# Optimization experiments

Measured on AMD Instinct MI355X. Metric: run time of the kernel, lower is better.

## Reference

```python
import jax, jax.numpy as jnp
import numpy as np

B, T, TAU = 4, 512, 512
D_MODEL = 1024  # in_dim == out_dim (required: pos embedding dim out_dim feeds pos_proj with in_size=in_dim)
H, D = 16, 64
LN_EPS = 1e-5


def rel_shift(x):
    # x: [B, T, L, H] -> Transformer-XL relative shift
    b, t, l, h = x.shape
    x = jnp.pad(x, ((0, 0), (0, 0), (1, 0), (0, 0)))  # pad j-dim front
    x = x.reshape(b, l + 1, t, h)[:, 1:, :, :]
    return x.reshape(b, t, l, h)


def setup_inputs() -> dict:
    key = jax.random.key(0)
    ks = jax.random.split(key, 7)
    s = 0.02
    return {
        "inputs": jax.random.normal(ks[0], (B, T, D_MODEL), jnp.float32),
        "memory": jax.random.normal(ks[1], (B, TAU, D_MODEL), jnp.float32),
        "w_qkv": jax.random.normal(ks[2], (3 * H * D, D_MODEL), jnp.float32) * s,
        "w_pos": jax.random.normal(ks[3], (H * D, D_MODEL), jnp.float32) * s,
        "w_out": jax.random.normal(ks[4], (D_MODEL, H * D), jnp.float32) * s,
        "uvar": jax.random.normal(ks[5], (H, D), jnp.float32) * s,
        "vvar": jax.random.normal(ks[6], (H, D), jnp.float32) * s,
        "ln_gamma": jnp.ones((D_MODEL,), jnp.float32),
        "ln_beta": jnp.zeros((D_MODEL,), jnp.float32),
    }


def reference(inputs, memory, w_qkv, w_pos, w_out, uvar, vvar, ln_gamma, ln_beta):
    b, t, din = inputs.shape
    tau = memory.shape[1]
    L = tau + t
    h, d = uvar.shape

    x = jnp.concatenate([jax.lax.stop_gradient(memory), inputs], axis=1)  # [B,L,Din]
    # input layernorm
    mu = jnp.mean(x, axis=-1, keepdims=True)
    var = jnp.mean((x - mu) ** 2, axis=-1, keepdims=True)
    x = (x - mu) / jnp.sqrt(var + LN_EPS) * ln_gamma + ln_beta

    qkv = x @ w_qkv.T  # [B,L,3HD]
    q, k, v = jnp.split(qkv, 3, axis=-1)
    q = q[:, -t:].reshape(b, t, h, d)
    k = k.reshape(b, L, h, d)
    v = v.reshape(b, L, h, d)

    # sinusoidal relative position embedding, dim = out_dim (= din here)
    inv_freq = 1.0 / (10000.0 ** (jnp.arange(0, din, 2, dtype=jnp.float32) / din))
    pos = jnp.arange(L - 1, -1, -1, dtype=jnp.float32)
    sin_in = pos[:, None] * inv_freq[None, :]                 # [L, din/2]
    phi = jnp.concatenate([jnp.sin(sin_in), jnp.cos(sin_in)], axis=-1)  # [L, din]
    R = (phi @ w_pos.T).reshape(L, h, d)

    score = jnp.einsum('bihd,bjhd->bijh', q + uvar, k)        # content score
    pos_score = jnp.einsum('bihd,jhd->bijh', q + vvar, R)     # position score
    score = (score + rel_shift(pos_score)) / (d ** 0.5)       # [B,T,L,H]

    # causal mask: query i attends to j <= tau + i
    mask = (jnp.arange(L)[None, :] <= (tau + jnp.arange(t))[:, None]).astype(score.dtype)
    mask = mask[None, :, :, None]
    masked = score * mask + 1e30 * (mask - 1.0)
    w = jax.nn.softmax(masked, axis=2)

    out = jnp.einsum('bijh,bjhd->bihd', w, v).reshape(b, t, h * d)
    return out @ w_out.T
```

## Files before the change

### kernel.cpp

```cpp
#include <hip/hip_runtime.h>
#include <math.h>

#define B_   4
#define T_   512
#define TAU_ 512
#define L_   1024
#define DM_  1024
#define H_   16
#define D_   64

typedef short  s16x8 __attribute__((ext_vector_type(8)));
typedef ushort u16x4 __attribute__((ext_vector_type(4)));
typedef float  f32x4 __attribute__((ext_vector_type(4)));

#define SC_LOG2 0.18033688011f

__device__ __forceinline__ ushort f2bf(float x) {
  uint u = __float_as_uint(x);
  u += 0x7fffu + ((u >> 16) & 1u);
  return (ushort)(u >> 16);
}
__device__ __forceinline__ float bf2f(ushort u) {
  return __uint_as_float(((uint)u) << 16);
}
__device__ __forceinline__ int sw64(int row, int col) {
  return row * 64 + (col ^ ((row & 7) << 3));
}

__global__ __launch_bounds__(256) void prep_kernel(
    const float* __restrict__ inp, const float* __restrict__ mem,
    const float* __restrict__ gamma, const float* __restrict__ beta,
    ushort* __restrict__ xn, ushort* __restrict__ phi,
    const float* __restrict__ wq, ushort* __restrict__ wqb,
    const float* __restrict__ wp, ushort* __restrict__ wpb,
    const float* __restrict__ wo, ushort* __restrict__ wob) {
  int blk = blockIdx.x;
  int t = threadIdx.x;
  if (blk < 4096) {
    int row = blk;
    int b = row >> 10, l = row & 1023;
    const float* src = (l < TAU_)
        ? mem + ((size_t)b * TAU_ + l) * DM_
        : inp + ((size_t)b * T_ + (l - TAU_)) * DM_;
    float4 v = *(const float4*)(src + t * 4);
    float s  = v.x + v.y + v.z + v.w;
    float s2 = v.x * v.x + v.y * v.y + v.z * v.z + v.w * v.w;
#pragma unroll
    for (int off = 32; off > 0; off >>= 1) {
      s  += __shfl_down(s, off);
      s2 += __shfl_down(s2, off);
    }
    __shared__ float red[8];
    __shared__ float stat[2];
    int wid = t >> 6;
    if ((t & 63) == 0) { red[wid * 2] = s; red[wid * 2 + 1] = s2; }
    __syncthreads();
    if (t == 0) {
      float ts  = red[0] + red[2] + red[4] + red[6];
      float ts2 = red[1] + red[3] + red[5] + red[7];
      float mu  = ts * (1.0f / DM_);
      float var = ts2 * (1.0f / DM_) - mu * mu;
      stat[0] = mu;
      stat[1] = 1.0f / sqrtf(var + 1e-5f);
    }
    __syncthreads();
    float mu = stat[0], rstd = stat[1];
    float4 g  = *(const float4*)(gamma + t * 4);
    float4 be = *(const float4*)(beta  + t * 4);
    u16x4 o;
    o[0] = f2bf((v.x - mu) * rstd * g.x + be.x);
    o[1] = f2bf((v.y - mu) * rstd * g.y + be.y);
    o[2] = f2bf((v.z - mu) * rstd * g.z + be.z);
    o[3] = f2bf((v.w - mu) * rstd * g.w + be.w);
    *(u16x4*)(xn + (size_t)row * DM_ + t * 4) = o;
  } else if (blk < 8192) {
    int idx = (blk - 4096) * 256 + t;
    int m = idx >> 10, c = idx & 1023;
    float p = (float)(1023 - m);
    int cc = (c < 512) ? c : c - 512;
    float invf = __expf(-((float)(2 * cc) * (1.0f / 1024.0f)) * 9.210340371976184f);
    float a = p * invf;
    phi[idx] = f2bf((c < 512) ? sinf(a) : cosf(a));
  } else {
    int i = (blk - 8192) * 256 + t;
    const float* src; ushort* dst; int off;
    if (i < 786432)       { src = wq; dst = wqb; off = i; }
    else if (i < 1048576) { src = wp; dst = wpb; off = i - 786432; }
    else                  { src = wo; dst = wob; off = i - 1048576; }
    float4 v = *(const float4*)(src + (size_t)off * 4);
    u16x4 o = { f2bf(v.x), f2bf(v.y), f2bf(v.z), f2bf(v.w) };
    *(u16x4*)(dst + (size_t)off * 4) = o;
  }
}

template <typename CT>
__device__ __forceinline__ void gemm_nt_body(
    const ushort* __restrict__ A, const ushort* __restrict__ B,
    CT* __restrict__ C, int M, int N, int K, int bx, int by) {
  __shared__ __attribute__((aligned(16))) ushort As[128 * 32];
  __shared__ __attribute__((aligned(16))) ushort Bs[128 * 32];
  int t = threadIdx.x;
  int w = t >> 6, lane = t & 63, g = lane >> 4, low = lane & 15;
  int wr = w >> 1, wc = w & 1;
  int m0 = by * 128, n0 = bx * 128;
  f32x4 acc[4][4] = {};

  for (int kt = 0; kt < K; kt += 32) {
    __syncthreads();
#pragma unroll
    for (int q = 0; q < 2; ++q) {
      int f = t + q * 256;
      int row = f >> 2;
      int gslot = (f & 3) ^ ((row >> 1) & 3);
      const ushort* ga = A + (size_t)(m0 + row) * K + kt + gslot * 8;
      const ushort* gb = B + (size_t)(n0 + row) * K + kt + gslot * 8;
      __builtin_amdgcn_global_load_lds(
          (const __attribute__((address_space(1))) void*)ga,
          (__attribute__((address_space(3))) void*)&As[(q * 256 + w * 64) * 8],
          16, 0, 0);
      __builtin_amdgcn_global_load_lds(
          (const __attribute__((address_space(1))) void*)gb,
          (__attribute__((address_space(3))) void*)&Bs[(q * 256 + w * 64) * 8],
          16, 0, 0);
    }
    __syncthreads();

    s16x8 af[4], bfr[4];
#pragma unroll
    for (int mi = 0; mi < 4; ++mi) {
      int row = wr * 64 + mi * 16 + low;
      af[mi] = *(const s16x8*)&As[row * 32 + ((g ^ ((row >> 1) & 3)) * 8)];
    }
#pragma unroll
    for (int ni = 0; ni < 4; ++ni) {
      int col = wc * 64 + ni * 16 + low;
      bfr[ni] = *(const s16x8*)&Bs[col * 32 + ((g ^ ((col >> 1) & 3)) * 8)];
    }
    __builtin_amdgcn_s_setprio(1);
#pragma unroll
    for (int mi = 0; mi < 4; ++mi)
#pragma unroll
      for (int ni = 0; ni < 4; ++ni)
        acc[mi][ni] = __builtin_amdgcn_mfma_f32_16x16x32_bf16(
            af[mi], bfr[ni], acc[mi][ni], 0, 0, 0);
    __builtin_amdgcn_s_setprio(0);
  }
#pragma unroll
  for (int mi = 0; mi < 4; ++mi)
#pragma unroll
    for (int ni = 0; ni < 4; ++ni)
#pragma unroll
      for (int r = 0; r < 4; ++r) {
        int m = m0 + wr * 64 + mi * 16 + 4 * g + r;
        int n = n0 + wc * 64 + ni * 16 + low;
        if constexpr (sizeof(CT) == 2)
          C[(size_t)m * N + n] = f2bf(acc[mi][ni][r]);
        else
          C[(size_t)m * N + n] = acc[mi][ni][r];
      }
}

__global__ __launch_bounds__(256) void qkv_r_gemm(
    const ushort* __restrict__ xnb, const ushort* __restrict__ wqb,
    ushort* __restrict__ qkvB,
    const ushort* __restrict__ phib, const ushort* __restrict__ wpb,
    ushort* __restrict__ RmB) {
  int id = blockIdx.x;
  if (id < 768)
    gemm_nt_body<ushort>(xnb, wqb, qkvB, 4096, 3072, 1024, id % 24, id / 24);
  else {
    id -= 768;
    gemm_nt_body<ushort>(phib, wpb, RmB, 1024, 1024, 1024, id % 8, id / 8);
  }
}

__global__ __launch_bounds__(256) void out_gemm(
    const ushort* __restrict__ attnb, const ushort* __restrict__ wob,
    float* __restrict__ out) {
  gemm_nt_body<float>(attnb, wob, out, 2048, 1024, 1024,
                      blockIdx.x % 8, blockIdx.x / 8);
}

__global__ __launch_bounds__(256) void vtrans_kernel(
    const ushort* __restrict__ qkv, ushort* __restrict__ vtg) {
  __shared__ ushort vs[64 * 65];
  int bid = blockIdx.x;
  int lt = bid & 15;
  int h  = (bid >> 4) & 15;
  int b  = bid >> 8;
  int l0 = lt * 64;
  int t = threadIdx.x;
#pragma unroll
  for (int q = 0; q < 2; ++q) {
    int c = t + q * 256;
    int row = c >> 3, sl = c & 7;
    s16x8 v = *(const s16x8*)(qkv +
        (size_t)(b * L_ + l0 + row) * 3072 + 2048 + h * 64 + sl * 8);
#pragma unroll
    for (int e = 0; e < 8; ++e) vs[row * 65 + sl * 8 + e] = (ushort)v[e];
  }
  __syncthreads();
#pragma unroll
  for (int q = 0; q < 2; ++q) {
    int c = t + q * 256;
    int d = c >> 3, sl = c & 7;
    s16x8 o;
#pragma unroll
    for (int e = 0; e < 8; ++e) o[e] = (short)vs[(sl * 8 + e) * 65 + d];
    *(s16x8*)(vtg + (size_t)((b * 16 + h) * 64 + d) * 1024 + l0 + sl * 8) = o;
  }
}

__global__ __launch_bounds__(256) void attn_mfma_kernel(
    const ushort* __restrict__ qkv, const ushort* __restrict__ Rm,
    const ushort* __restrict__ vtg,
    const float* __restrict__ uvar, const float* __restrict__ vvar,
    ushort* __restrict__ attn) {
  __shared__ __attribute__((aligned(16))) ushort Ks[2][64 * 64];
  __shared__ __attribute__((aligned(16))) ushort Vt[2][64 * 64];
  __shared__ __attribute__((aligned(16))) ushort Rs[2][128 * 64];
  __shared__ __attribute__((aligned(16))) ushort Pp[4][16 * 64];

  int t   = threadIdx.x;
  int w   = t >> 6;
  int lw  = t & 63;
  int g   = lw >> 4;
  int low = lw & 15;

  int bid = blockIdx.x;
  int bi_r = bid & 7;
  int h   = (bid >> 3) & 15;
  int b   = bid >> 7;
  int bi  = (h & 1) ? (7 - bi_r) : bi_r;
  int i0  = bi * 64;
  int lb_w = 48 - 16 * w;

  auto stage = [&](int buf, int tl) {
    int j0s = tl * 64;
#pragma unroll
    for (int q = 0; q < 2; ++q) {
      int c = t + q * 256;
      int row = c >> 3;
      int sl = (c & 7) ^ (row & 7);
      const ushort* srck = qkv + (size_t)(b * L_ + j0s + row) * 3072 +
                           1024 + h * 64 + sl * 8;
      __builtin_amdgcn_global_load_lds(
          (const __attribute__((address_space(1))) void*)srck,
          (__attribute__((address_space(3))) void*)&Ks[buf][(q * 256 + w * 64) * 8],
          16, 0, 0);
      const ushort* srcv = vtg + (size_t)((b * 16 + h) * 64 + row) * 1024 +
                           j0s + sl * 8;
      __builtin_amdgcn_global_load_lds(
          (const __attribute__((address_space(1))) void*)srcv,
          (__attribute__((address_space(3))) void*)&Vt[buf][(q * 256 + w * 64) * 8],
          16, 0, 0);
    }
    int mb = j0s + 448 - i0;
#pragma unroll
    for (int q = 0; q < 4; ++q) {
      int c = t + q * 256;
      int row = c >> 3;
      int m = mb + row; m = (m > 1023) ? 1023 : m;
      int sl = (c & 7) ^ (row & 7);
      const ushort* srcr = Rm + (size_t)m * 1024 + h * 64 + sl * 8;
      __builtin_amdgcn_global_load_lds(
          (const __attribute__((address_space(1))) void*)srcr,
          (__attribute__((address_space(3))) void*)&Rs[buf][(q * 256 + w * 64) * 8],
          16, 0, 0);
    }
  };

  int iq = i0 + 16 * w + low;
  s16x8 qu[2], qv[2];
  {
    const ushort* qrow = qkv + (size_t)(b * L_ + TAU_ + iq) * 3072 + h * 64;
    const float* ur = uvar + h * 64;
    const float* vr = vvar + h * 64;
#pragma unroll
    for (int kc = 0; kc < 2; ++kc) {
      int dbase = kc * 32 + 8 * g;
#pragma unroll
      for (int e = 0; e < 8; ++e) {
        float q = bf2f(qrow[dbase + e]);
        qu[kc][e] = (short)f2bf(q + ur[dbase + e]);
        qv[kc][e] = (short)f2bf(q + vr[dbase + e]);
      }
    }
  }

  f32x4 O[4] = {};
  float mreg[4] = {-INFINITY, -INFINITY, -INFINITY, -INFINITY};
  float lreg[4] = {0.f, 0.f, 0.f, 0.f};

  int ntiles = 9 + bi;
  stage(0, 0);
  __syncthreads();
  int cur = 0;
  for (int tile = 0; tile < ntiles; ++tile) {
    int j0 = tile * 64;
    if (tile + 1 < ntiles) stage(cur ^ 1, tile + 1);

    f32x4 s[4] = {};
    f32x4 p[5] = {};
    __builtin_amdgcn_s_setprio(1);
#pragma unroll
    for (int jt = 0; jt < 4; ++jt) {
#pragma unroll
      for (int kc = 0; kc < 2; ++kc) {
        s16x8 kb = *(const s16x8*)&Ks[cur][sw64(jt * 16 + low, kc * 32 + 8 * g)];
        s[jt] = __builtin_amdgcn_mfma_f32_16x16x32_bf16(qu[kc], kb, s[jt], 0, 0, 0);
      }
    }
#pragma unroll
    for (int mt = 0; mt < 5; ++mt) {
#pragma unroll
      for (int kc = 0; kc < 2; ++kc) {
        s16x8 rb = *(const s16x8*)&Rs[cur][sw64(lb_w + mt * 16 + low, kc * 32 + 8 * g)];
        p[mt] = __builtin_amdgcn_mfma_f32_16x16x32_bf16(qv[kc], rb, p[mt], 0, 0, 0);
      }
    }
    __builtin_amdgcn_s_setprio(0);

    bool fullvalid = (j0 + 63 <= TAU_ + i0 + 16 * w);
#pragma unroll
    for (int r = 0; r < 4; ++r) {
      int iL = 4 * g + r;
      int src = g * 16 + ((low + 15 - iL) & 15);
      float sh0 = __shfl(p[0][r], src);
      float sh1 = __shfl(p[1][r], src);
      float sh2 = __shfl(p[2][r], src);
      float sh3 = __shfl(p[3][r], src);
      float sh4 = __shfl(p[4][r], src);
      bool lo = (low <= iL);
      float po0 = lo ? sh0 : sh1;
      float po1 = lo ? sh1 : sh2;
      float po2 = lo ? sh2 : sh3;
      float po3 = lo ? sh3 : sh4;
      if (fullvalid) {
        s[0][r] = (s[0][r] + po0) * SC_LOG2;
        s[1][r] = (s[1][r] + po1) * SC_LOG2;
        s[2][r] = (s[2][r] + po2) * SC_LOG2;
        s[3][r] = (s[3][r] + po3) * SC_LOG2;
      } else {
        int lim = TAU_ + i0 + 16 * w + iL;
        s[0][r] = (j0 +  0 + low <= lim) ? (s[0][r] + po0) * SC_LOG2 : -1e30f;
        s[1][r] = (j0 + 16 + low <= lim) ? (s[1][r] + po1) * SC_LOG2 : -1e30f;
        s[2][r] = (j0 + 32 + low <= lim) ? (s[2][r] + po2) * SC_LOG2 : -1e30f;
        s[3][r] = (j0 + 48 + low <= lim) ? (s[3][r] + po3) * SC_LOG2 : -1e30f;
      }
    }
#pragma unroll
    for (int r = 0; r < 4; ++r) {
      float mx = fmaxf(fmaxf(s[0][r], s[1][r]), fmaxf(s[2][r], s[3][r]));
      mx = fmaxf(mx, __shfl_xor(mx, 1));
      mx = fmaxf(mx, __shfl_xor(mx, 2));
      mx = fmaxf(mx, __shfl_xor(mx, 4));
      mx = fmaxf(mx, __shfl_xor(mx, 8));
      float mn = fmaxf(mreg[r], mx);
      float alpha = exp2f(mreg[r] - mn);
      mreg[r] = mn;
      float sum = 0.f;
#pragma unroll
      for (int jt = 0; jt < 4; ++jt) {
        float pe = exp2f(s[jt][r] - mn);
        s[jt][r] = pe;
        sum += pe;
      }
      sum += __shfl_xor(sum, 1);
      sum += __shfl_xor(sum, 2);
      sum += __shfl_xor(sum, 4);
      sum += __shfl_xor(sum, 8);
      lreg[r] = lreg[r] * alpha + sum;
      O[0][r] *= alpha; O[1][r] *= alpha; O[2][r] *= alpha; O[3][r] *= alpha;
    }
#pragma unroll
    for (int jt = 0; jt < 4; ++jt)
#pragma unroll
      for (int r = 0; r < 4; ++r)
        Pp[w][sw64(4 * g + r, jt * 16 + low)] = f2bf(s[jt][r]);
    asm volatile("s_waitcnt lgkmcnt(0)" ::: "memory");
    s16x8 pa0 = *(const s16x8*)&Pp[w][sw64(low, 8 * g)];
    s16x8 pa1 = *(const s16x8*)&Pp[w][sw64(low, 32 + 8 * g)];
    __builtin_amdgcn_s_setprio(1);
#pragma unroll
    for (int dt = 0; dt < 4; ++dt) {
      s16x8 v0 = *(const s16x8*)&Vt[cur][sw64(dt * 16 + low, 8 * g)];
      s16x8 v1 = *(const s16x8*)&Vt[cur][sw64(dt * 16 + low, 32 + 8 * g)];
      O[dt] = __builtin_amdgcn_mfma_f32_16x16x32_bf16(pa0, v0, O[dt], 0, 0, 0);
      O[dt] = __builtin_amdgcn_mfma_f32_16x16x32_bf16(pa1, v1, O[dt], 0, 0, 0);
    }
    __builtin_amdgcn_s_setprio(0);
    __syncthreads();
    cur ^= 1;
  }
  float inv[4];
#pragma unroll
  for (int r = 0; r < 4; ++r) inv[r] = 1.0f / lreg[r];
#pragma unroll
  for (int dt = 0; dt < 4; ++dt)
#pragma unroll
    for (int r = 0; r < 4; ++r)
      attn[((size_t)(b * T_ + i0 + 16 * w + 4 * g + r)) * 1024 +
           h * 64 + dt * 16 + low] = f2bf(O[dt][r] * inv[r]);
}

extern "C" void kernel_launch(void* const* d_in, const int* in_sizes, int n_in,
                              void* d_out, int out_size, void* d_ws, size_t ws_size,
                              hipStream_t stream) {
  const float* inputs = (const float*)d_in[0];
  const float* memory = (const float*)d_in[1];
  const float* w_qkv  = (const float*)d_in[2];
  const float* w_pos  = (const float*)d_in[3];
  const float* w_out  = (const float*)d_in[4];
  const float* uvar   = (const float*)d_in[5];
  const float* vvar   = (const float*)d_in[6];
  const float* gamma  = (const float*)d_in[7];
  const float* beta   = (const float*)d_in[8];
  float* out = (float*)d_out;

  ushort* qkvB = (ushort*)d_ws;
  ushort* xnb  = qkvB + (size_t)4096 * 3072;
  ushort* phib = xnb  + (size_t)4096 * 1024;
  ushort* RmB  = phib + (size_t)1024 * 1024;
  ushort* wqb  = RmB  + (size_t)1024 * 1024;
  ushort* wpb  = wqb  + (size_t)3072 * 1024;
  ushort* wob  = wpb  + (size_t)1024 * 1024;
  ushort* vtg  = wob  + (size_t)1024 * 1024;
  ushort* attnb = xnb;

  prep_kernel<<<13312, 256, 0, stream>>>(inputs, memory, gamma, beta, xnb,
                                         phib, w_qkv, wqb, w_pos, wpb, w_out, wob);
  qkv_r_gemm<<<832, 256, 0, stream>>>(xnb, wqb, qkvB, phib, wpb, RmB);
  vtrans_kernel<<<B_ * H_ * 16, 256, 0, stream>>>(qkvB, vtg);
  attn_mfma_kernel<<<dim3(B_ * H_ * 8), 256, 0, stream>>>(qkvB, RmB, vtg, uvar, vvar, attnb);
  out_gemm<<<128, 256, 0, stream>>>(attnb, wob, out);
}
```

Before: 229.4 us.

## Load R directly to registers, remap block ids, drop setprio hints

The attention kernel stops staging the relative-position matrix R through shared memory and has each wave load its R fragments straight from global memory into registers. This removes the R shared-memory buffers and their staging traffic, and it adds a launch bound targeting higher occupancy. Block-index remapping is added to the GEMMs and to the attention kernel to change how work is spread across XCDs. The odd/even head causal-balance swap and the s_setprio hints are removed. Global R loads now sit on each tile's critical path with less reuse between waves, and the remap may change load balance.

```diff
diff --git a/kernel.cpp b/kernel.cpp
--- a/kernel.cpp
+++ b/kernel.cpp
@@ -136,14 +136,12 @@
       int col = wc * 64 + ni * 16 + low;
       bfr[ni] = *(const s16x8*)&Bs[col * 32 + ((g ^ ((col >> 1) & 3)) * 8)];
     }
-    __builtin_amdgcn_s_setprio(1);
 #pragma unroll
     for (int mi = 0; mi < 4; ++mi)
 #pragma unroll
       for (int ni = 0; ni < 4; ++ni)
         acc[mi][ni] = __builtin_amdgcn_mfma_f32_16x16x32_bf16(
             af[mi], bfr[ni], acc[mi][ni], 0, 0, 0);
-    __builtin_amdgcn_s_setprio(0);
   }
 #pragma unroll
   for (int mi = 0; mi < 4; ++mi)
@@ -165,7 +163,8 @@
     ushort* __restrict__ qkvB,
     const ushort* __restrict__ phib, const ushort* __restrict__ wpb,
     ushort* __restrict__ RmB) {
-  int id = blockIdx.x;
+  int orig = blockIdx.x;
+  int id = (orig & 7) * 104 + (orig >> 3);
   if (id < 768)
     gemm_nt_body<ushort>(xnb, wqb, qkvB, 4096, 3072, 1024, id % 24, id / 24);
   else {
@@ -177,8 +176,9 @@
 __global__ __launch_bounds__(256) void out_gemm(
     const ushort* __restrict__ attnb, const ushort* __restrict__ wob,
     float* __restrict__ out) {
-  gemm_nt_body<float>(attnb, wob, out, 2048, 1024, 1024,
-                      blockIdx.x % 8, blockIdx.x / 8);
+  int orig = blockIdx.x;
+  int id = (orig & 7) * 16 + (orig >> 3);
+  gemm_nt_body<float>(attnb, wob, out, 2048, 1024, 1024, id % 8, id / 8);
 }
 
 __global__ __launch_bounds__(256) void vtrans_kernel(
@@ -211,14 +211,13 @@
   }
 }
 
-__global__ __launch_bounds__(256) void attn_mfma_kernel(
+__global__ __launch_bounds__(256, 4) void attn_mfma_kernel(
     const ushort* __restrict__ qkv, const ushort* __restrict__ Rm,
     const ushort* __restrict__ vtg,
     const float* __restrict__ uvar, const float* __restrict__ vvar,
     ushort* __restrict__ attn) {
   __shared__ __attribute__((aligned(16))) ushort Ks[2][64 * 64];
   __shared__ __attribute__((aligned(16))) ushort Vt[2][64 * 64];
-  __shared__ __attribute__((aligned(16))) ushort Rs[2][128 * 64];
   __shared__ __attribute__((aligned(16))) ushort Pp[4][16 * 64];
 
   int t   = threadIdx.x;
@@ -227,11 +226,11 @@
   int g   = lw >> 4;
   int low = lw & 15;
 
-  int bid = blockIdx.x;
-  int bi_r = bid & 7;
+  int orig = blockIdx.x;
+  int bid  = (orig & 7) * 64 + (orig >> 3);
+  int bi  = bid & 7;
   int h   = (bid >> 3) & 15;
   int b   = bid >> 7;
-  int bi  = (h & 1) ? (7 - bi_r) : bi_r;
   int i0  = bi * 64;
   int lb_w = 48 - 16 * w;
 
@@ -255,19 +254,6 @@
           (__attribute__((address_space(3))) void*)&Vt[buf][(q * 256 + w * 64) * 8],
           16, 0, 0);
     }
-    int mb = j0s + 448 - i0;
-#pragma unroll
-    for (int q = 0; q < 4; ++q) {
-      int c = t + q * 256;
-      int row = c >> 3;
-      int m = mb + row; m = (m > 1023) ? 1023 : m;
-      int sl = (c & 7) ^ (row & 7);
-      const ushort* srcr = Rm + (size_t)m * 1024 + h * 64 + sl * 8;
-      __builtin_amdgcn_global_load_lds(
-          (const __attribute__((address_space(1))) void*)srcr,
-          (__attribute__((address_space(3))) void*)&Rs[buf][(q * 256 + w * 64) * 8],
-          16, 0, 0);
-    }
   };
 
   int iq = i0 + 16 * w + low;
@@ -300,9 +286,19 @@
     int j0 = tile * 64;
     if (tile + 1 < ntiles) stage(cur ^ 1, tile + 1);
 
+    int mb = j0 + 448 - i0;
+    s16x8 rb[10];
+#pragma unroll
+    for (int kc = 0; kc < 2; ++kc)
+#pragma unroll
+      for (int mt = 0; mt < 5; ++mt) {
+        int m = mb + lb_w + mt * 16 + low;
+        m = (m > 1023) ? 1023 : m;
+        rb[kc * 5 + mt] = *(const s16x8*)(Rm + (size_t)m * 1024 + h * 64 +
+                                          kc * 32 + 8 * g);
+      }
+
     f32x4 s[4] = {};
-    f32x4 p[5] = {};
-    __builtin_amdgcn_s_setprio(1);
 #pragma unroll
     for (int jt = 0; jt < 4; ++jt) {
 #pragma unroll
@@ -311,15 +307,13 @@
         s[jt] = __builtin_amdgcn_mfma_f32_16x16x32_bf16(qu[kc], kb, s[jt], 0, 0, 0);
       }
     }
-#pragma unroll
-    for (int mt = 0; mt < 5; ++mt) {
-#pragma unroll
-      for (int kc = 0; kc < 2; ++kc) {
-        s16x8 rb = *(const s16x8*)&Rs[cur][sw64(lb_w + mt * 16 + low, kc * 32 + 8 * g)];
-        p[mt] = __builtin_amdgcn_mfma_f32_16x16x32_bf16(qv[kc], rb, p[mt], 0, 0, 0);
-      }
-    }
-    __builtin_amdgcn_s_setprio(0);
+    f32x4 p[5] = {};
+#pragma unroll
+    for (int kc = 0; kc < 2; ++kc)
+#pragma unroll
+      for (int mt = 0; mt < 5; ++mt)
+        p[mt] = __builtin_amdgcn_mfma_f32_16x16x32_bf16(
+            qv[kc], rb[kc * 5 + mt], p[mt], 0, 0, 0);
 
     bool fullvalid = (j0 + 63 <= TAU_ + i0 + 16 * w);
 #pragma unroll
@@ -381,7 +375,6 @@
     asm volatile("s_waitcnt lgkmcnt(0)" ::: "memory");
     s16x8 pa0 = *(const s16x8*)&Pp[w][sw64(low, 8 * g)];
     s16x8 pa1 = *(const s16x8*)&Pp[w][sw64(low, 32 + 8 * g)];
-    __builtin_amdgcn_s_setprio(1);
 #pragma unroll
     for (int dt = 0; dt < 4; ++dt) {
       s16x8 v0 = *(const s16x8*)&Vt[cur][sw64(dt * 16 + low, 8 * g)];
@@ -389,7 +382,6 @@
       O[dt] = __builtin_amdgcn_mfma_f32_16x16x32_bf16(pa0, v0, O[dt], 0, 0, 0);
       O[dt] = __builtin_amdgcn_mfma_f32_16x16x32_bf16(pa1, v1, O[dt], 0, 0, 0);
     }
-    __builtin_amdgcn_s_setprio(0);
     __syncthreads();
     cur ^= 1;
   }
```

Result: slower. 267.4 us (+16.6%).

## Deepen GEMM K-tile to 64, remap GEMM blocks, simplify attention softmax path

Applied to the files above, without the earlier changes.

The shared GEMM body now stages a 64-wide K slice per iteration with an 8-way XOR swizzle, halving the number of barrier pairs. Block indices in both GEMM launches are permuted so neighbouring blocks are spread across XCDs. In attention, the head-parity reversal of query-block order, the s_setprio hints, and the fully-valid fast path for masking are removed, and exp2 with a folded log2 scale is replaced by __expf with a plain 0.125 scale. This mixes GEMM tiling changes with what looks like a partial revert of earlier attention micro-optimisations, and it doubles the GEMM LDS footprint.

```diff
diff --git a/kernel.cpp b/kernel.cpp
--- a/kernel.cpp
+++ b/kernel.cpp
@@ -12,8 +12,6 @@
 typedef short  s16x8 __attribute__((ext_vector_type(8)));
 typedef ushort u16x4 __attribute__((ext_vector_type(4)));
 typedef float  f32x4 __attribute__((ext_vector_type(4)));
-
-#define SC_LOG2 0.18033688011f
 
 __device__ __forceinline__ ushort f2bf(float x) {
   uint u = __float_as_uint(x);
@@ -97,21 +95,21 @@
 __device__ __forceinline__ void gemm_nt_body(
     const ushort* __restrict__ A, const ushort* __restrict__ B,
     CT* __restrict__ C, int M, int N, int K, int bx, int by) {
-  __shared__ __attribute__((aligned(16))) ushort As[128 * 32];
-  __shared__ __attribute__((aligned(16))) ushort Bs[128 * 32];
+  __shared__ __attribute__((aligned(16))) ushort As[128 * 64];
+  __shared__ __attribute__((aligned(16))) ushort Bs[128 * 64];
   int t = threadIdx.x;
   int w = t >> 6, lane = t & 63, g = lane >> 4, low = lane & 15;
   int wr = w >> 1, wc = w & 1;
   int m0 = by * 128, n0 = bx * 128;
   f32x4 acc[4][4] = {};
 
-  for (int kt = 0; kt < K; kt += 32) {
+  for (int kt = 0; kt < K; kt += 64) {
     __syncthreads();
 #pragma unroll
-    for (int q = 0; q < 2; ++q) {
-      int f = t + q * 256;
-      int row = f >> 2;
-      int gslot = (f & 3) ^ ((row >> 1) & 3);
+    for (int q = 0; q < 4; ++q) {
+      int c = t + q * 256;
+      int row = c >> 3;
+      int gslot = (c & 7) ^ (row & 7);
       const ushort* ga = A + (size_t)(m0 + row) * K + kt + gslot * 8;
       const ushort* gb = B + (size_t)(n0 + row) * K + kt + gslot * 8;
       __builtin_amdgcn_global_load_lds(
@@ -125,25 +123,26 @@
     }
     __syncthreads();
 
-    s16x8 af[4], bfr[4];
-#pragma unroll
-    for (int mi = 0; mi < 4; ++mi) {
-      int row = wr * 64 + mi * 16 + low;
-      af[mi] = *(const s16x8*)&As[row * 32 + ((g ^ ((row >> 1) & 3)) * 8)];
-    }
-#pragma unroll
-    for (int ni = 0; ni < 4; ++ni) {
-      int col = wc * 64 + ni * 16 + low;
-      bfr[ni] = *(const s16x8*)&Bs[col * 32 + ((g ^ ((col >> 1) & 3)) * 8)];
-    }
-    __builtin_amdgcn_s_setprio(1);
-#pragma unroll
-    for (int mi = 0; mi < 4; ++mi)
-#pragma unroll
-      for (int ni = 0; ni < 4; ++ni)
-        acc[mi][ni] = __builtin_amdgcn_mfma_f32_16x16x32_bf16(
-            af[mi], bfr[ni], acc[mi][ni], 0, 0, 0);
-    __builtin_amdgcn_s_setprio(0);
+#pragma unroll
+    for (int kc = 0; kc < 2; ++kc) {
+      s16x8 af[4], bfr[4];
+#pragma unroll
+      for (int mi = 0; mi < 4; ++mi) {
+        int row = wr * 64 + mi * 16 + low;
+        af[mi] = *(const s16x8*)&As[row * 64 + (((4 * kc + g) ^ (row & 7)) * 8)];
+      }
+#pragma unroll
+      for (int ni = 0; ni < 4; ++ni) {
+        int col = wc * 64 + ni * 16 + low;
+        bfr[ni] = *(const s16x8*)&Bs[col * 64 + (((4 * kc + g) ^ (col & 7)) * 8)];
+      }
+#pragma unroll
+      for (int mi = 0; mi < 4; ++mi)
+#pragma unroll
+        for (int ni = 0; ni < 4; ++ni)
+          acc[mi][ni] = __builtin_amdgcn_mfma_f32_16x16x32_bf16(
+              af[mi], bfr[ni], acc[mi][ni], 0, 0, 0);
+    }
   }
 #pragma unroll
   for (int mi = 0; mi < 4; ++mi)
@@ -165,7 +164,8 @@
     ushort* __restrict__ qkvB,
     const ushort* __restrict__ phib, const ushort* __restrict__ wpb,
     ushort* __restrict__ RmB) {
-  int id = blockIdx.x;
+  int orig = blockIdx.x;
+  int id = (orig & 7) * 104 + (orig >> 3);
   if (id < 768)
     gemm_nt_body<ushort>(xnb, wqb, qkvB, 4096, 3072, 1024, id % 24, id / 24);
   else {
@@ -177,8 +177,9 @@
 __global__ __launch_bounds__(256) void out_gemm(
     const ushort* __restrict__ attnb, const ushort* __restrict__ wob,
     float* __restrict__ out) {
-  gemm_nt_body<float>(attnb, wob, out, 2048, 1024, 1024,
-                      blockIdx.x % 8, blockIdx.x / 8);
+  int orig = blockIdx.x;
+  int id = (orig & 7) * 16 + (orig >> 3);
+  gemm_nt_body<float>(attnb, wob, out, 2048, 1024, 1024, id % 8, id / 8);
 }
 
 __global__ __launch_bounds__(256) void vtrans_kernel(
@@ -228,10 +229,9 @@
   int low = lw & 15;
 
   int bid = blockIdx.x;
-  int bi_r = bid & 7;
+  int bi  = bid & 7;
   int h   = (bid >> 3) & 15;
   int b   = bid >> 7;
-  int bi  = (h & 1) ? (7 - bi_r) : bi_r;
   int i0  = bi * 64;
   int lb_w = 48 - 16 * w;
 
@@ -301,8 +301,6 @@
     if (tile + 1 < ntiles) stage(cur ^ 1, tile + 1);
 
     f32x4 s[4] = {};
-    f32x4 p[5] = {};
-    __builtin_amdgcn_s_setprio(1);
 #pragma unroll
     for (int jt = 0; jt < 4; ++jt) {
 #pragma unroll
@@ -311,6 +309,7 @@
         s[jt] = __builtin_amdgcn_mfma_f32_16x16x32_bf16(qu[kc], kb, s[jt], 0, 0, 0);
       }
     }
+    f32x4 p[5] = {};
 #pragma unroll
     for (int mt = 0; mt < 5; ++mt) {
 #pragma unroll
@@ -319,9 +318,6 @@
         p[mt] = __builtin_amdgcn_mfma_f32_16x16x32_bf16(qv[kc], rb, p[mt], 0, 0, 0);
       }
     }
-    __builtin_amdgcn_s_setprio(0);
-
-    bool fullvalid = (j0 + 63 <= TAU_ + i0 + 16 * w);
 #pragma unroll
     for (int r = 0; r < 4; ++r) {
       int iL = 4 * g + r;
@@ -336,18 +332,11 @@
       float po1 = lo ? sh1 : sh2;
       float po2 = lo ? sh2 : sh3;
       float po3 = lo ? sh3 : sh4;
-      if (fullvalid) {
-        s[0][r] = (s[0][r] + po0) * SC_LOG2;
-        s[1][r] = (s[1][r] + po1) * SC_LOG2;
-        s[2][r] = (s[2][r] + po2) * SC_LOG2;
-        s[3][r] = (s[3][r] + po3) * SC_LOG2;
-      } else {
-        int lim = TAU_ + i0 + 16 * w + iL;
-        s[0][r] = (j0 +  0 + low <= lim) ? (s[0][r] + po0) * SC_LOG2 : -1e30f;
-        s[1][r] = (j0 + 16 + low <= lim) ? (s[1][r] + po1) * SC_LOG2 : -1e30f;
-        s[2][r] = (j0 + 32 + low <= lim) ? (s[2][r] + po2) * SC_LOG2 : -1e30f;
-        s[3][r] = (j0 + 48 + low <= lim) ? (s[3][r] + po3) * SC_LOG2 : -1e30f;
-      }
+      int lim = TAU_ + i0 + 16 * w + iL;
+      s[0][r] = (j0 +  0 + low <= lim) ? (s[0][r] + po0) * 0.125f : -1e30f;
+      s[1][r] = (j0 + 16 + low <= lim) ? (s[1][r] + po1) * 0.125f : -1e30f;
+      s[2][r] = (j0 + 32 + low <= lim) ? (s[2][r] + po2) * 0.125f : -1e30f;
+      s[3][r] = (j0 + 48 + low <= lim) ? (s[3][r] + po3) * 0.125f : -1e30f;
     }
 #pragma unroll
     for (int r = 0; r < 4; ++r) {
@@ -357,12 +346,12 @@
       mx = fmaxf(mx, __shfl_xor(mx, 4));
       mx = fmaxf(mx, __shfl_xor(mx, 8));
       float mn = fmaxf(mreg[r], mx);
-      float alpha = exp2f(mreg[r] - mn);
+      float alpha = __expf(mreg[r] - mn);
       mreg[r] = mn;
       float sum = 0.f;
 #pragma unroll
       for (int jt = 0; jt < 4; ++jt) {
-        float pe = exp2f(s[jt][r] - mn);
+        float pe = __expf(s[jt][r] - mn);
         s[jt][r] = pe;
         sum += pe;
       }
@@ -381,7 +370,6 @@
     asm volatile("s_waitcnt lgkmcnt(0)" ::: "memory");
     s16x8 pa0 = *(const s16x8*)&Pp[w][sw64(low, 8 * g)];
     s16x8 pa1 = *(const s16x8*)&Pp[w][sw64(low, 32 + 8 * g)];
-    __builtin_amdgcn_s_setprio(1);
 #pragma unroll
     for (int dt = 0; dt < 4; ++dt) {
       s16x8 v0 = *(const s16x8*)&Vt[cur][sw64(dt * 16 + low, 8 * g)];
@@ -389,7 +377,6 @@
       O[dt] = __builtin_amdgcn_mfma_f32_16x16x32_bf16(pa0, v0, O[dt], 0, 0, 0);
       O[dt] = __builtin_amdgcn_mfma_f32_16x16x32_bf16(pa1, v1, O[dt], 0, 0, 0);
     }
-    __builtin_amdgcn_s_setprio(0);
     __syncthreads();
     cur ^= 1;
   }
```

After: 212.1 us. 7.5% less time.
